# Performance work log

Hardware: AMD Instinct MI355X
Metric: run time of the kernel (lower is better)

The kernel has to match this reference:

```python
import jax, jax.numpy as jnp
import numpy as np

N_NODES = 2000
C_IN = 64
G_DIMS = [1, 256, 256, 256]
C_EMB = 128
HAZ = 512


def setup_inputs() -> dict:
    key = jax.random.key(0)
    ks = jax.random.split(key, 16)
    B, E = 128, 64000
    inp = jax.random.normal(ks[0], (B, C_IN + N_NODES), dtype=jnp.float32)
    src = jax.random.randint(ks[1], (E,), 0, N_NODES, dtype=jnp.int32)
    dst = jax.random.randint(ks[2], (E,), 0, N_NODES, dtype=jnp.int32)
    def lin(k, fi, fo):
        return jax.random.normal(k, (fi, fo), dtype=jnp.float32) / np.sqrt(fi)
    params = {
        'W0': lin(ks[3], G_DIMS[0], G_DIMS[1]), 'b0': jnp.zeros((G_DIMS[1],), jnp.float32),
        'W1': lin(ks[4], G_DIMS[1], G_DIMS[2]), 'b1': jnp.zeros((G_DIMS[2],), jnp.float32),
        'W2': lin(ks[5], G_DIMS[2], G_DIMS[3]), 'b2': jnp.zeros((G_DIMS[3],), jnp.float32),
        'We': lin(ks[6], C_IN, C_EMB),
        'Wh1': lin(ks[7], 2 * G_DIMS[3] + C_EMB, HAZ), 'bh1': jnp.zeros((HAZ,), jnp.float32),
        'Wh2': lin(ks[8], HAZ, HAZ // 2), 'bh2': jnp.zeros((HAZ // 2,), jnp.float32),
        'Wh3': lin(ks[9], HAZ // 2, 1),
    }
    return dict(inp=inp, src=src, dst=dst, **params)


def _gcn_layer(x, src, dst, dout_is, din_is, W, b):
    # x: [B, N, d_in]; DGL GraphConv norm='both': D_out^-1/2 gather-sum D_in^-1/2, then XW+b
    B, N, _ = x.shape
    h = x * dout_is[None, :, None]
    msg = h[:, src, :]                                   # [B, E, d_in]
    agg = jnp.zeros_like(h).at[:, dst, :].add(msg)       # scatter-add over edges
    agg = agg * din_is[None, :, None]
    return agg @ W + b


def reference(inp, src, dst, W0, b0, W1, b1, W2, b2, We, Wh1, bh1, Wh2, bh2, Wh3):
    B = inp.shape[0]
    inp_c = inp[:, :C_IN]
    x = inp[:, C_IN:].reshape(B, N_NODES, 1)
    # degree normalizers (DGL clamps degree to min 1)
    ones = jnp.ones_like(src, dtype=jnp.float32)
    dout = jnp.maximum(jnp.zeros((N_NODES,), jnp.float32).at[src].add(ones), 1.0)
    din = jnp.maximum(jnp.zeros((N_NODES,), jnp.float32).at[dst].add(ones), 1.0)
    dout_is = jax.lax.rsqrt(dout)
    din_is = jax.lax.rsqrt(din)

    embed = jax.nn.relu(inp_c @ We)
    hg = 0.0
    for W, b in ((W0, b0), (W1, b1), (W2, b2)):
        x = jax.nn.relu(_gcn_layer(x, src, dst, dout_is, din_is, W, b))
        r = jnp.concatenate([x.mean(axis=1), x.max(axis=1)], axis=-1)  # avg|max readout
        hg = hg + jax.nn.relu(r)

    fusion = jnp.concatenate([embed, hg], axis=1)
    h = jax.nn.relu(fusion @ Wh1 + bh1)
    h = jax.nn.relu(h @ Wh2 + bh2)
    out = h @ Wh3  # out_dim == 1 -> Identity head (dropout=0 / eval)
    return out
```

## Files before the change

### kernel.cpp

```cpp
#include <hip/hip_runtime.h>
#include <hip/hip_bf16.h>

#define B_    128
#define NN    2000
#define C_    256
#define E_    64000
#define CIN   64
#define ROWST 2064
#define CEMB  128
#define HAZ1  512
#define HAZ2  256
#define FUSD  640

typedef unsigned short u16;
typedef __attribute__((ext_vector_type(8))) short short8;
typedef __attribute__((ext_vector_type(8))) unsigned short ush8;
typedef __attribute__((ext_vector_type(4))) float f32x4;

static constexpr size_t OFF_DEGO = 0;
static constexpr size_t OFF_DEGI = 8000;
static constexpr size_t OFF_CUR  = 16000;
static constexpr size_t OFF_WOUT = 24000;
static constexpr size_t OFF_WIN  = 32000;
static constexpr size_t OFF_IOFF = 40000;
static constexpr size_t OFF_CSRC = 48192;
static constexpr size_t OFF_CSRW = 304192;
static constexpr size_t OFF_HG   = 560192;
static constexpr size_t OFF_EMB  = 822336;
static constexpr size_t OFF_H1   = 887872;
static constexpr size_t OFF_H2   = 1150016;
static constexpr size_t OFF_PSUM = 1281088;
static constexpr size_t OFF_PMAX = 1412160;
static constexpr size_t OFF_A    = 1543232;
static constexpr size_t OFF_WT1H = 2567232;
static constexpr size_t OFF_WT2H = 2829376;
static constexpr size_t OFF_XBUF = 4194304;

__device__ __forceinline__ u16 f2bf(float f) {
    union { float f; unsigned u; } v; v.f = f;
    unsigned u = v.u;
    unsigned r = (u + 0x7FFFu + ((u >> 16) & 1u)) >> 16;
    return (u16)r;
}
__device__ __forceinline__ float bf2f(u16 h) {
    union { unsigned u; float f; } v; v.u = ((unsigned)h) << 16;
    return v.f;
}

__global__ void k_zero(float* p, int n) {
    int i = blockIdx.x * 256 + threadIdx.x;
    if (i < n) p[i] = 0.f;
}

__global__ void k_deg(const int* __restrict__ src, const int* __restrict__ dst,
                      int* __restrict__ dego, int* __restrict__ degi) {
    int e = blockIdx.x * 256 + threadIdx.x;
    if (e < E_) {
        atomicAdd(&dego[src[e]], 1);
        atomicAdd(&degi[dst[e]], 1);
    }
}

__global__ void k_norm(const int* __restrict__ dego, const int* __restrict__ degi,
                       float* __restrict__ wout, float* __restrict__ win) {
    int n = blockIdx.x * 256 + threadIdx.x;
    if (n < NN) {
        wout[n] = rsqrtf(fmaxf((float)dego[n], 1.f));
        win[n]  = rsqrtf(fmaxf((float)degi[n], 1.f));
    }
}

__global__ void k_scan(const int* __restrict__ degi, int* __restrict__ ioff) {
    __shared__ int part[512];
    int t = threadIdx.x;
    int base = t * 4;
    int v[4]; int s = 0;
#pragma unroll
    for (int i = 0; i < 4; i++) {
        int idx = base + i;
        v[i] = (idx < NN) ? degi[idx] : 0;
        s += v[i];
    }
    part[t] = s;
    __syncthreads();
    for (int o = 1; o < 512; o <<= 1) {
        int x = 0;
        if (t >= o) x = part[t - o];
        __syncthreads();
        part[t] += x;
        __syncthreads();
    }
    int run = (t == 0) ? 0 : part[t - 1];
#pragma unroll
    for (int i = 0; i < 4; i++) {
        int idx = base + i;
        if (idx <= NN) ioff[idx] = run;
        run += v[i];
    }
}

__global__ void k_fill(const int* __restrict__ src, const int* __restrict__ dst,
                       const float* __restrict__ wout, const float* __restrict__ win,
                       const int* __restrict__ ioff, int* __restrict__ cursor,
                       int* __restrict__ csrc, float* __restrict__ csrw) {
    int e = blockIdx.x * 256 + threadIdx.x;
    if (e < E_) {
        int d = dst[e];
        int s = src[e];
        int p = atomicAdd(&cursor[d], 1);
        int i = ioff[d] + p;
        csrc[i] = s;
        csrw[i] = wout[s] * win[d];
    }
}

__global__ __launch_bounds__(256) void k_prepw(const float* __restrict__ W,
                                               u16* __restrict__ Th) {
    int n = blockIdx.x, k = threadIdx.x;
    Th[n * 256 + k] = f2bf(W[(size_t)k * 256 + n]);
}

__global__ __launch_bounds__(64) void k_agg_scalar(
        const float* __restrict__ inp, const int* __restrict__ ioff,
        const int* __restrict__ csrc, const float* __restrict__ csrw,
        float* __restrict__ a) {
    int n = blockIdx.x * 64 + threadIdx.x;
    int b = blockIdx.y;
    if (n >= NN) return;
    const float* row = inp + (size_t)b * ROWST + CIN;
    int e0 = ioff[n], e1 = ioff[n + 1];
    float acc = 0.f;
    for (int i = e0; i < e1; i++) acc += csrw[i] * row[csrc[i]];
    a[(size_t)b * NN + n] = acc;
}

__global__ __launch_bounds__(256) void k_pool0(
        const float* __restrict__ a, const float* __restrict__ W0,
        const float* __restrict__ b0, float* __restrict__ hg) {
    int b = blockIdx.x, c = threadIdx.x;
    float w0c = W0[c], b0c = b0[c];
    const float* ab = a + (size_t)b * NN;
    float s = 0.f, mx = 0.f;
    for (int n = 0; n < NN; n++) {
        float v = fmaxf(fmaf(ab[n], w0c, b0c), 0.f);
        s += v;
        mx = fmaxf(mx, v);
    }
    hg[(size_t)b * 512 + c]       += s * (1.f / (float)NN);
    hg[(size_t)b * 512 + 256 + c] += mx;
}

__global__ __launch_bounds__(64) void k_agg_l1(
        const float* __restrict__ a, const int* __restrict__ ioff,
        const int* __restrict__ csrc, const float* __restrict__ csrw,
        const float* __restrict__ W0, const float* __restrict__ b0,
        u16* __restrict__ xout, int b0g) {
    int n = blockIdx.x, bp = blockIdx.y, t = threadIdx.x;
    int half = t >> 5, c8 = (t & 31) * 8;
    int bl = bp * 2 + half;
    int e0 = ioff[n], e1 = ioff[n + 1];
    const float* ab = a + (size_t)(b0g + bl) * NN;
    float w[8], bb[8], acca[8] = {}, accb[8] = {};
#pragma unroll
    for (int j = 0; j < 8; j++) { w[j] = W0[c8 + j]; bb[j] = b0[c8 + j]; }
    int i = e0;
    for (; i + 2 <= e1; i += 2) {
        float a0 = ab[csrc[i]],     we0 = csrw[i];
        float a1 = ab[csrc[i + 1]], we1 = csrw[i + 1];
#pragma unroll
        for (int j = 0; j < 8; j++) {
            acca[j] = fmaf(fmaxf(fmaf(a0, w[j], bb[j]), 0.f), we0, acca[j]);
            accb[j] = fmaf(fmaxf(fmaf(a1, w[j], bb[j]), 0.f), we1, accb[j]);
        }
    }
    if (i < e1) {
        float a0 = ab[csrc[i]], we0 = csrw[i];
#pragma unroll
        for (int j = 0; j < 8; j++)
            acca[j] = fmaf(fmaxf(fmaf(a0, w[j], bb[j]), 0.f), we0, acca[j]);
    }
    ush8 o;
#pragma unroll
    for (int j = 0; j < 8; j++) o[j] = f2bf(acca[j] + accb[j]);
    *reinterpret_cast<ush8*>(&xout[((size_t)bl * NN + n) * C_ + c8]) = o;
}

__global__ __launch_bounds__(64) void k_agg_bf(
        const u16* __restrict__ xin, const int* __restrict__ ioff,
        const int* __restrict__ csrc, const float* __restrict__ csrw,
        u16* __restrict__ xout, int QBH) {
    int l = blockIdx.x + NN * blockIdx.y;
    int xcd = l & 7, slot = l >> 3;
    int q = slot / NN;
    int bp = xcd * QBH + q;
    int n = slot - q * NN;
    int t = threadIdx.x;
    int half = t >> 5, c8 = (t & 31) * 8;
    int bl = bp * 2 + half;
    int e0 = ioff[n], e1 = ioff[n + 1];
    const u16* xb = xin + (size_t)bl * NN * C_ + c8;
    float acca[8] = {}, accb[8] = {};
    int i = e0;
    for (; i + 2 <= e1; i += 2) {
        int s0 = csrc[i];     float w0 = csrw[i];
        int s1 = csrc[i + 1]; float w1 = csrw[i + 1];
        ush8 v0 = *reinterpret_cast<const ush8*>(&xb[(size_t)s0 * C_]);
        ush8 v1 = *reinterpret_cast<const ush8*>(&xb[(size_t)s1 * C_]);
#pragma unroll
        for (int j = 0; j < 8; j++) {
            acca[j] = fmaf(bf2f(v0[j]), w0, acca[j]);
            accb[j] = fmaf(bf2f(v1[j]), w1, accb[j]);
        }
    }
    if (i < e1) {
        int s0 = csrc[i]; float w0 = csrw[i];
        ush8 v0 = *reinterpret_cast<const ush8*>(&xb[(size_t)s0 * C_]);
#pragma unroll
        for (int j = 0; j < 8; j++) acca[j] = fmaf(bf2f(v0[j]), w0, acca[j]);
    }
    ush8 o;
#pragma unroll
    for (int j = 0; j < 8; j++) o[j] = f2bf(acca[j] + accb[j]);
    *reinterpret_cast<ush8*>(&xout[((size_t)bl * NN + n) * C_ + c8]) = o;
}

#define GM 128
#define GN 128
#define GK 32
#define LDP 40

template<int OUT>
__global__ __launch_bounds__(256) void k_gemm_mfma(
        const u16* __restrict__ Abf, const u16* __restrict__ WTh,
        const float* __restrict__ bias,
        u16* __restrict__ Cbf, float* __restrict__ psum, float* __restrict__ pmax) {
    __shared__ u16 Ah[GM * LDP];
    __shared__ u16 Bh[GN * LDP];
    __shared__ float lsum[2][2][GN];
    __shared__ float lmax[2][2][GN];
    int tid  = threadIdx.x;
    int lane = tid & 63, wave = tid >> 6;
    int wm = wave >> 1, wn = wave & 1;
    int n0 = blockIdx.x * GN;
    int m0 = blockIdx.y * GM;
    int blk = lane >> 4, rr = lane & 15;

    f32x4 acc[4][4] = {};

    for (int k0 = 0; k0 < 256; k0 += GK) {
#pragma unroll
        for (int q = 0; q < 2; q++) {
            int f = tid + 256 * q;
            int row = f >> 2, seg = f & 3;
            ush8 va = *reinterpret_cast<const ush8*>(
                &Abf[(size_t)(m0 + row) * 256 + k0 + seg * 8]);
            ush8 vb = *reinterpret_cast<const ush8*>(
                &WTh[(size_t)(n0 + row) * 256 + k0 + seg * 8]);
            *reinterpret_cast<ush8*>(&Ah[row * LDP + seg * 8]) = va;
            *reinterpret_cast<ush8*>(&Bh[row * LDP + seg * 8]) = vb;
        }
        __syncthreads();

        short8 af[4], bf[4];
#pragma unroll
        for (int mr = 0; mr < 4; mr++)
            af[mr] = *reinterpret_cast<const short8*>(
                &Ah[(wm * 64 + mr * 16 + rr) * LDP + blk * 8]);
#pragma unroll
        for (int nr = 0; nr < 4; nr++)
            bf[nr] = *reinterpret_cast<const short8*>(
                &Bh[(wn * 64 + nr * 16 + rr) * LDP + blk * 8]);
#pragma unroll
        for (int mr = 0; mr < 4; mr++)
#pragma unroll
            for (int nr = 0; nr < 4; nr++)
                acc[mr][nr] = __builtin_amdgcn_mfma_f32_16x16x32_bf16(
                    af[mr], bf[nr], acc[mr][nr], 0, 0, 0);
        __syncthreads();
    }

    int bl0   = m0 / NN;
    int split = (bl0 + 1) * NN - m0;

    float s_lo[4] = {}, s_hi[4] = {}, m_lo[4] = {}, m_hi[4] = {};
#pragma unroll
    for (int nr = 0; nr < 4; nr++) {
        int col = n0 + wn * 64 + nr * 16 + rr;
        float bs = bias[col];
#pragma unroll
        for (int mr = 0; mr < 4; mr++) {
            int rl = wm * 64 + mr * 16 + blk * 4;
#pragma unroll
            for (int j = 0; j < 4; j++) {
                float v = fmaxf(acc[mr][nr][j] + bs, 0.f);
                if (OUT == 1)
                    Cbf[(size_t)(m0 + rl + j) * 256 + col] = f2bf(v);
                bool second = (rl + j) >= split;
                s_lo[nr] += second ? 0.f : v;
                s_hi[nr] += second ? v : 0.f;
                m_lo[nr] = second ? m_lo[nr] : fmaxf(m_lo[nr], v);
                m_hi[nr] = second ? fmaxf(m_hi[nr], v) : m_hi[nr];
            }
        }
    }
#pragma unroll
    for (int nr = 0; nr < 4; nr++) {
        s_lo[nr] += __shfl_xor(s_lo[nr], 16); s_lo[nr] += __shfl_xor(s_lo[nr], 32);
        s_hi[nr] += __shfl_xor(s_hi[nr], 16); s_hi[nr] += __shfl_xor(s_hi[nr], 32);
        m_lo[nr] = fmaxf(m_lo[nr], __shfl_xor(m_lo[nr], 16));
        m_lo[nr] = fmaxf(m_lo[nr], __shfl_xor(m_lo[nr], 32));
        m_hi[nr] = fmaxf(m_hi[nr], __shfl_xor(m_hi[nr], 16));
        m_hi[nr] = fmaxf(m_hi[nr], __shfl_xor(m_hi[nr], 32));
    }
    if (lane < 16) {
#pragma unroll
        for (int nr = 0; nr < 4; nr++) {
            int cl = wn * 64 + nr * 16 + lane;
            lsum[0][wm][cl] = s_lo[nr];
            lsum[1][wm][cl] = s_hi[nr];
            lmax[0][wm][cl] = m_lo[nr];
            lmax[1][wm][cl] = m_hi[nr];
        }
    }
    __syncthreads();
    {
        int seg = tid >> 7, cl = tid & 127;
        if (!(seg == 1 && split >= GM)) {
            float s = lsum[seg][0][cl] + lsum[seg][1][cl];
            float m = fmaxf(lmax[seg][0][cl], lmax[seg][1][cl]);
            int blx = bl0 + seg;
            atomicAdd(&psum[blx * C_ + n0 + cl], s);
            atomicMax((unsigned int*)&pmax[blx * C_ + n0 + cl], __float_as_uint(m));
        }
    }
}

__global__ __launch_bounds__(256) void k_pool_combine(
        float* __restrict__ psum, float* __restrict__ pmax,
        float* __restrict__ hg, int b0g) {
    int bl = blockIdx.x, c = threadIdx.x;
    float s = psum[bl * C_ + c];
    float m = pmax[bl * C_ + c];
    psum[bl * C_ + c] = 0.f;
    pmax[bl * C_ + c] = 0.f;
    size_t b = b0g + bl;
    hg[b * 512 + c]       += s * (1.f / (float)NN);
    hg[b * 512 + 256 + c] += m;
}

__global__ __launch_bounds__(128) void k_embed(
        const float* __restrict__ inp, const float* __restrict__ We,
        float* __restrict__ emb) {
    int b = blockIdx.x, c = threadIdx.x;
    const float* row = inp + (size_t)b * ROWST;
    float a = 0.f;
    for (int k = 0; k < CIN; k++) a += row[k] * We[k * CEMB + c];
    emb[b * CEMB + c] = fmaxf(a, 0.f);
}

__global__ __launch_bounds__(512) void k_mlp1(
        const float* __restrict__ emb, const float* __restrict__ hg,
        const float* __restrict__ Wh1, const float* __restrict__ bh1,
        float* __restrict__ h1) {
    __shared__ float fus[FUSD];
    int b = blockIdx.x, j = threadIdx.x;
    if (j < CEMB) fus[j] = emb[b * CEMB + j];
    fus[CEMB + j] = hg[(size_t)b * 512 + j];
    __syncthreads();
    float a = bh1[j];
    for (int k = 0; k < FUSD; k++) a += fus[k] * Wh1[(size_t)k * HAZ1 + j];
    h1[(size_t)b * HAZ1 + j] = fmaxf(a, 0.f);
}

__global__ __launch_bounds__(256) void k_mlp2(
        const float* __restrict__ h1, const float* __restrict__ Wh2,
        const float* __restrict__ bh2, float* __restrict__ h2) {
    __shared__ float f2[HAZ1];
    int b = blockIdx.x, j = threadIdx.x;
    f2[j]       = h1[(size_t)b * HAZ1 + j];
    f2[256 + j] = h1[(size_t)b * HAZ1 + 256 + j];
    __syncthreads();
    float a = bh2[j];
    for (int k = 0; k < HAZ1; k++) a += f2[k] * Wh2[(size_t)k * HAZ2 + j];
    h2[(size_t)b * HAZ2 + j] = fmaxf(a, 0.f);
}

__global__ __launch_bounds__(256) void k_out(
        const float* __restrict__ h2, const float* __restrict__ Wh3,
        float* __restrict__ out) {
    __shared__ float red[256];
    int b = blockIdx.x, t = threadIdx.x;
    red[t] = h2[(size_t)b * HAZ2 + t] * Wh3[t];
    __syncthreads();
    for (int o = 128; o > 0; o >>= 1) {
        if (t < o) red[t] += red[t + o];
        __syncthreads();
    }
    if (t == 0) out[b] = red[0];
}

extern "C" void kernel_launch(void* const* d_in, const int* in_sizes, int n_in,
                              void* d_out, int out_size, void* d_ws, size_t ws_size,
                              hipStream_t stream) {
    const float* inp = (const float*)d_in[0];
    const int*   src = (const int*)d_in[1];
    const int*   dst = (const int*)d_in[2];
    const float* W0  = (const float*)d_in[3];
    const float* b0  = (const float*)d_in[4];
    const float* W1  = (const float*)d_in[5];
    const float* b1  = (const float*)d_in[6];
    const float* W2  = (const float*)d_in[7];
    const float* b2  = (const float*)d_in[8];
    const float* We  = (const float*)d_in[9];
    const float* Wh1 = (const float*)d_in[10];
    const float* bh1 = (const float*)d_in[11];
    const float* Wh2 = (const float*)d_in[12];
    const float* bh2 = (const float*)d_in[13];
    const float* Wh3 = (const float*)d_in[14];
    float* out = (float*)d_out;

    char* ws = (char*)d_ws;
    int*   dego = (int*)(ws + OFF_DEGO);
    int*   degi = (int*)(ws + OFF_DEGI);
    int*   cur  = (int*)(ws + OFF_CUR);
    float* wout = (float*)(ws + OFF_WOUT);
    float* win  = (float*)(ws + OFF_WIN);
    int*   ioff = (int*)(ws + OFF_IOFF);
    int*   csrc = (int*)(ws + OFF_CSRC);
    float* csrw = (float*)(ws + OFF_CSRW);
    float* hg   = (float*)(ws + OFF_HG);
    float* emb  = (float*)(ws + OFF_EMB);
    float* h1   = (float*)(ws + OFF_H1);
    float* h2   = (float*)(ws + OFF_H2);
    float* psum = (float*)(ws + OFF_PSUM);
    float* pmax = (float*)(ws + OFF_PMAX);
    float* avec = (float*)(ws + OFF_A);
    u16*   wt1h = (u16*)(ws + OFF_WT1H);
    u16*   wt2h = (u16*)(ws + OFF_WT2H);

    const size_t perb = (size_t)NN * C_ * 4;
    int CB = 128;
    while (CB > 16 && OFF_XBUF + (size_t)CB * perb > ws_size) CB >>= 1;
    int nchunk = B_ / CB;
    int CBH = CB / 2;
    int QBH = CBH / 8;

    u16* xB   = (u16*)(ws + OFF_XBUF);
    u16* xAbf = (u16*)(ws + OFF_XBUF + (size_t)CB * NN * C_ * 2);

    k_zero<<<dim3((6000 + 255) / 256), 256, 0, stream>>>((float*)dego, 6000);
    k_zero<<<dim3((65536 + 255) / 256), 256, 0, stream>>>(hg, 65536);
    k_zero<<<dim3((65536 + 255) / 256), 256, 0, stream>>>(psum, 65536);

    k_deg<<<dim3((E_ + 255) / 256), 256, 0, stream>>>(src, dst, dego, degi);
    k_norm<<<dim3((NN + 255) / 256), 256, 0, stream>>>(dego, degi, wout, win);
    k_scan<<<1, 512, 0, stream>>>(degi, ioff);
    k_fill<<<dim3((E_ + 255) / 256), 256, 0, stream>>>(src, dst, wout, win, ioff, cur, csrc, csrw);
    k_prepw<<<256, 256, 0, stream>>>(W1, wt1h);
    k_prepw<<<256, 256, 0, stream>>>(W2, wt2h);

    k_agg_scalar<<<dim3((NN + 63) / 64, B_), 64, 0, stream>>>(inp, ioff, csrc, csrw, avec);
    k_pool0<<<B_, 256, 0, stream>>>(avec, W0, b0, hg);

    dim3 gridNB(NN, CBH);
    dim3 gridGemm(C_ / GN, (CB * NN) / GM);

    for (int c = 0; c < nchunk; ++c) {
        int b0g = c * CB;

        k_agg_l1<<<gridNB, 64, 0, stream>>>(avec, ioff, csrc, csrw, W0, b0, xB, b0g);
        k_gemm_mfma<1><<<gridGemm, 256, 0, stream>>>(xB, wt1h, b1, xAbf, psum, pmax);
        k_pool_combine<<<CB, 256, 0, stream>>>(psum, pmax, hg, b0g);

        k_agg_bf<<<gridNB, 64, 0, stream>>>(xAbf, ioff, csrc, csrw, xB, QBH);
        k_gemm_mfma<0><<<gridGemm, 256, 0, stream>>>(xB, wt2h, b2, nullptr, psum, pmax);
        k_pool_combine<<<CB, 256, 0, stream>>>(psum, pmax, hg, b0g);
    }

    k_embed<<<B_, 128, 0, stream>>>(inp, We, emb);
    k_mlp1<<<B_, 512, 0, stream>>>(emb, hg, Wh1, bh1, h1);
    k_mlp2<<<B_, 256, 0, stream>>>(h1, Wh2, bh2, h2);
    k_out<<<B_, 256, 0, stream>>>(h2, Wh3, out);
}
```

Before: 645.2 us.

## Fuse small kernels, transpose input for aggregation, prefetch GEMM tiles, unroll gather

Merges the zero, norm/scan, prepw, embed/mlp and out kernels into fewer launches. It transposes the node input to node-major [N,B] so scalar aggregation and layer-1 gathers read coalesced across the batch. The bf16 aggregation loop is unrolled to four edges, and the MFMA GEMM register-prefetches the next K tile while computing the current one. These target launch overhead, uncoalesced gathers and memory latency, at the cost of an extra transpose kernel and workspace buffer.

```diff
diff --git a/kernel.cpp b/kernel.cpp
--- a/kernel.cpp
+++ b/kernel.cpp
@@ -26,14 +26,13 @@
 static constexpr size_t OFF_CSRC = 48192;
 static constexpr size_t OFF_CSRW = 304192;
 static constexpr size_t OFF_HG   = 560192;
-static constexpr size_t OFF_EMB  = 822336;
 static constexpr size_t OFF_H1   = 887872;
-static constexpr size_t OFF_H2   = 1150016;
 static constexpr size_t OFF_PSUM = 1281088;
 static constexpr size_t OFF_PMAX = 1412160;
 static constexpr size_t OFF_A    = 1543232;
 static constexpr size_t OFF_WT1H = 2567232;
 static constexpr size_t OFF_WT2H = 2829376;
+static constexpr size_t OFF_XT   = 3091520;
 static constexpr size_t OFF_XBUF = 4194304;
 
 __device__ __forceinline__ u16 f2bf(float f) {
@@ -47,9 +46,12 @@
     return v.f;
 }
 
-__global__ void k_zero(float* p, int n) {
+__global__ void k_init(int* __restrict__ deg3, float* __restrict__ hg,
+                       float* __restrict__ ps) {
     int i = blockIdx.x * 256 + threadIdx.x;
-    if (i < n) p[i] = 0.f;
+    if (i < 6000) deg3[i] = 0;
+    else if (i < 6000 + 65536) hg[i - 6000] = 0.f;
+    else if (i < 6000 + 131072) ps[i - 71536] = 0.f;
 }
 
 __global__ void k_deg(const int* __restrict__ src, const int* __restrict__ dst,
@@ -61,16 +63,9 @@
     }
 }
 
-__global__ void k_norm(const int* __restrict__ dego, const int* __restrict__ degi,
-                       float* __restrict__ wout, float* __restrict__ win) {
-    int n = blockIdx.x * 256 + threadIdx.x;
-    if (n < NN) {
-        wout[n] = rsqrtf(fmaxf((float)dego[n], 1.f));
-        win[n]  = rsqrtf(fmaxf((float)degi[n], 1.f));
-    }
-}
-
-__global__ void k_scan(const int* __restrict__ degi, int* __restrict__ ioff) {
+__global__ void k_scan_norm(const int* __restrict__ degi, const int* __restrict__ dego,
+                            int* __restrict__ ioff, float* __restrict__ wout,
+                            float* __restrict__ win) {
     __shared__ int part[512];
     int t = threadIdx.x;
     int base = t * 4;
@@ -79,6 +74,10 @@
     for (int i = 0; i < 4; i++) {
         int idx = base + i;
         v[i] = (idx < NN) ? degi[idx] : 0;
+        if (idx < NN) {
+            wout[idx] = rsqrtf(fmaxf((float)dego[idx], 1.f));
+            win[idx]  = rsqrtf(fmaxf((float)v[i], 1.f));
+        }
         s += v[i];
     }
     part[t] = s;
@@ -114,35 +113,61 @@
     }
 }
 
-__global__ __launch_bounds__(256) void k_prepw(const float* __restrict__ W,
-                                               u16* __restrict__ Th) {
-    int n = blockIdx.x, k = threadIdx.x;
-    Th[n * 256 + k] = f2bf(W[(size_t)k * 256 + n]);
-}
-
-__global__ __launch_bounds__(64) void k_agg_scalar(
-        const float* __restrict__ inp, const int* __restrict__ ioff,
+__global__ __launch_bounds__(256) void k_prepw2(
+        const float* __restrict__ W1, const float* __restrict__ W2,
+        u16* __restrict__ T1, u16* __restrict__ T2) {
+    int which = blockIdx.x >> 8;
+    int n = blockIdx.x & 255, k = threadIdx.x;
+    const float* W = which ? W2 : W1;
+    u16* T = which ? T2 : T1;
+    T[n * 256 + k] = f2bf(W[(size_t)k * 256 + n]);
+}
+
+__global__ __launch_bounds__(256) void k_xt(
+        const float* __restrict__ inp, float* __restrict__ xT) {
+    __shared__ float tl[32][33];
+    int tx = threadIdx.x & 31, ty = threadIdx.x >> 5;
+    int n0 = blockIdx.x * 32, b0 = blockIdx.y * 32;
+#pragma unroll
+    for (int r = 0; r < 4; r++) {
+        int b = b0 + ty + r * 8;
+        int n = n0 + tx;
+        if (n < NN) tl[tx][ty + r * 8] = inp[(size_t)b * ROWST + CIN + n];
+    }
+    __syncthreads();
+#pragma unroll
+    for (int r = 0; r < 4; r++) {
+        int n = n0 + ty + r * 8;
+        int b = b0 + tx;
+        if (n < NN) xT[(size_t)n * B_ + b] = tl[ty + r * 8][tx];
+    }
+}
+
+__global__ __launch_bounds__(64) void k_agg_scalar_t(
+        const float* __restrict__ xT, const int* __restrict__ ioff,
         const int* __restrict__ csrc, const float* __restrict__ csrw,
-        float* __restrict__ a) {
-    int n = blockIdx.x * 64 + threadIdx.x;
-    int b = blockIdx.y;
-    if (n >= NN) return;
-    const float* row = inp + (size_t)b * ROWST + CIN;
+        float* __restrict__ aT) {
+    int n = blockIdx.x;
+    int b = blockIdx.y * 64 + threadIdx.x;
     int e0 = ioff[n], e1 = ioff[n + 1];
-    float acc = 0.f;
-    for (int i = e0; i < e1; i++) acc += csrw[i] * row[csrc[i]];
-    a[(size_t)b * NN + n] = acc;
+    float acc0 = 0.f, acc1 = 0.f;
+    int i = e0;
+    for (; i + 2 <= e1; i += 2) {
+        acc0 = fmaf(csrw[i],     xT[(size_t)csrc[i] * B_ + b],     acc0);
+        acc1 = fmaf(csrw[i + 1], xT[(size_t)csrc[i + 1] * B_ + b], acc1);
+    }
+    if (i < e1) acc0 = fmaf(csrw[i], xT[(size_t)csrc[i] * B_ + b], acc0);
+    aT[(size_t)n * B_ + b] = acc0 + acc1;
 }
 
 __global__ __launch_bounds__(256) void k_pool0(
-        const float* __restrict__ a, const float* __restrict__ W0,
+        const float* __restrict__ aT, const float* __restrict__ W0,
         const float* __restrict__ b0, float* __restrict__ hg) {
     int b = blockIdx.x, c = threadIdx.x;
     float w0c = W0[c], b0c = b0[c];
-    const float* ab = a + (size_t)b * NN;
     float s = 0.f, mx = 0.f;
     for (int n = 0; n < NN; n++) {
-        float v = fmaxf(fmaf(ab[n], w0c, b0c), 0.f);
+        float v = fmaxf(fmaf(aT[(size_t)n * B_ + b], w0c, b0c), 0.f);
         s += v;
         mx = fmaxf(mx, v);
     }
@@ -151,22 +176,30 @@
 }
 
 __global__ __launch_bounds__(64) void k_agg_l1(
-        const float* __restrict__ a, const int* __restrict__ ioff,
+        const float* __restrict__ aT, const int* __restrict__ ioff,
         const int* __restrict__ csrc, const float* __restrict__ csrw,
         const float* __restrict__ W0, const float* __restrict__ b0,
         u16* __restrict__ xout, int b0g) {
     int n = blockIdx.x, bp = blockIdx.y, t = threadIdx.x;
     int half = t >> 5, c8 = (t & 31) * 8;
     int bl = bp * 2 + half;
+    int bg = b0g + bl;
     int e0 = ioff[n], e1 = ioff[n + 1];
-    const float* ab = a + (size_t)(b0g + bl) * NN;
     float w[8], bb[8], acca[8] = {}, accb[8] = {};
-#pragma unroll
-    for (int j = 0; j < 8; j++) { w[j] = W0[c8 + j]; bb[j] = b0[c8 + j]; }
+    {
+        float4 w0 = *reinterpret_cast<const float4*>(&W0[c8]);
+        float4 w1 = *reinterpret_cast<const float4*>(&W0[c8 + 4]);
+        float4 v0 = *reinterpret_cast<const float4*>(&b0[c8]);
+        float4 v1 = *reinterpret_cast<const float4*>(&b0[c8 + 4]);
+        w[0]=w0.x; w[1]=w0.y; w[2]=w0.z; w[3]=w0.w;
+        w[4]=w1.x; w[5]=w1.y; w[6]=w1.z; w[7]=w1.w;
+        bb[0]=v0.x; bb[1]=v0.y; bb[2]=v0.z; bb[3]=v0.w;
+        bb[4]=v1.x; bb[5]=v1.y; bb[6]=v1.z; bb[7]=v1.w;
+    }
     int i = e0;
     for (; i + 2 <= e1; i += 2) {
-        float a0 = ab[csrc[i]],     we0 = csrw[i];
-        float a1 = ab[csrc[i + 1]], we1 = csrw[i + 1];
+        float a0 = aT[(size_t)csrc[i] * B_ + bg],     we0 = csrw[i];
+        float a1 = aT[(size_t)csrc[i + 1] * B_ + bg], we1 = csrw[i + 1];
 #pragma unroll
         for (int j = 0; j < 8; j++) {
             acca[j] = fmaf(fmaxf(fmaf(a0, w[j], bb[j]), 0.f), we0, acca[j]);
@@ -174,7 +207,7 @@
         }
     }
     if (i < e1) {
-        float a0 = ab[csrc[i]], we0 = csrw[i];
+        float a0 = aT[(size_t)csrc[i] * B_ + bg], we0 = csrw[i];
 #pragma unroll
         for (int j = 0; j < 8; j++)
             acca[j] = fmaf(fmaxf(fmaf(a0, w[j], bb[j]), 0.f), we0, acca[j]);
@@ -199,20 +232,26 @@
     int bl = bp * 2 + half;
     int e0 = ioff[n], e1 = ioff[n + 1];
     const u16* xb = xin + (size_t)bl * NN * C_ + c8;
-    float acca[8] = {}, accb[8] = {};
+    float acca[8] = {}, accb[8] = {}, accc[8] = {}, accd[8] = {};
     int i = e0;
-    for (; i + 2 <= e1; i += 2) {
+    for (; i + 4 <= e1; i += 4) {
         int s0 = csrc[i];     float w0 = csrw[i];
         int s1 = csrc[i + 1]; float w1 = csrw[i + 1];
+        int s2 = csrc[i + 2]; float w2 = csrw[i + 2];
+        int s3 = csrc[i + 3]; float w3 = csrw[i + 3];
         ush8 v0 = *reinterpret_cast<const ush8*>(&xb[(size_t)s0 * C_]);
         ush8 v1 = *reinterpret_cast<const ush8*>(&xb[(size_t)s1 * C_]);
+        ush8 v2 = *reinterpret_cast<const ush8*>(&xb[(size_t)s2 * C_]);
+        ush8 v3 = *reinterpret_cast<const ush8*>(&xb[(size_t)s3 * C_]);
 #pragma unroll
         for (int j = 0; j < 8; j++) {
             acca[j] = fmaf(bf2f(v0[j]), w0, acca[j]);
             accb[j] = fmaf(bf2f(v1[j]), w1, accb[j]);
-        }
-    }
-    if (i < e1) {
+            accc[j] = fmaf(bf2f(v2[j]), w2, accc[j]);
+            accd[j] = fmaf(bf2f(v3[j]), w3, accd[j]);
+        }
+    }
+    for (; i < e1; ++i) {
         int s0 = csrc[i]; float w0 = csrw[i];
         ush8 v0 = *reinterpret_cast<const ush8*>(&xb[(size_t)s0 * C_]);
 #pragma unroll
@@ -220,7 +259,8 @@
     }
     ush8 o;
 #pragma unroll
-    for (int j = 0; j < 8; j++) o[j] = f2bf(acca[j] + accb[j]);
+    for (int j = 0; j < 8; j++)
+        o[j] = f2bf((acca[j] + accb[j]) + (accc[j] + accd[j]));
     *reinterpret_cast<ush8*>(&xout[((size_t)bl * NN + n) * C_ + c8]) = o;
 }
 
@@ -244,23 +284,30 @@
     int n0 = blockIdx.x * GN;
     int m0 = blockIdx.y * GM;
     int blk = lane >> 4, rr = lane & 15;
+    int sr0 = tid >> 2, sseg = (tid & 3) * 8;
+    int sr1 = sr0 + 64;
 
     f32x4 acc[4][4] = {};
 
-    for (int k0 = 0; k0 < 256; k0 += GK) {
-#pragma unroll
-        for (int q = 0; q < 2; q++) {
-            int f = tid + 256 * q;
-            int row = f >> 2, seg = f & 3;
-            ush8 va = *reinterpret_cast<const ush8*>(
-                &Abf[(size_t)(m0 + row) * 256 + k0 + seg * 8]);
-            ush8 vb = *reinterpret_cast<const ush8*>(
-                &WTh[(size_t)(n0 + row) * 256 + k0 + seg * 8]);
-            *reinterpret_cast<ush8*>(&Ah[row * LDP + seg * 8]) = va;
-            *reinterpret_cast<ush8*>(&Bh[row * LDP + seg * 8]) = vb;
-        }
+    ush8 va0 = *reinterpret_cast<const ush8*>(&Abf[(size_t)(m0 + sr0) * 256 + sseg]);
+    ush8 vb0 = *reinterpret_cast<const ush8*>(&WTh[(size_t)(n0 + sr0) * 256 + sseg]);
+    ush8 va1 = *reinterpret_cast<const ush8*>(&Abf[(size_t)(m0 + sr1) * 256 + sseg]);
+    ush8 vb1 = *reinterpret_cast<const ush8*>(&WTh[(size_t)(n0 + sr1) * 256 + sseg]);
+
+#pragma unroll
+    for (int kk = 0; kk < 8; kk++) {
+        *reinterpret_cast<ush8*>(&Ah[sr0 * LDP + sseg]) = va0;
+        *reinterpret_cast<ush8*>(&Bh[sr0 * LDP + sseg]) = vb0;
+        *reinterpret_cast<ush8*>(&Ah[sr1 * LDP + sseg]) = va1;
+        *reinterpret_cast<ush8*>(&Bh[sr1 * LDP + sseg]) = vb1;
         __syncthreads();
-
+        if (kk < 7) {
+            int k0n = (kk + 1) * GK;
+            va0 = *reinterpret_cast<const ush8*>(&Abf[(size_t)(m0 + sr0) * 256 + k0n + sseg]);
+            vb0 = *reinterpret_cast<const ush8*>(&WTh[(size_t)(n0 + sr0) * 256 + k0n + sseg]);
+            va1 = *reinterpret_cast<const ush8*>(&Abf[(size_t)(m0 + sr1) * 256 + k0n + sseg]);
+            vb1 = *reinterpret_cast<const ush8*>(&WTh[(size_t)(n0 + sr1) * 256 + k0n + sseg]);
+        }
         short8 af[4], bf[4];
 #pragma unroll
         for (int mr = 0; mr < 4; mr++)
@@ -348,23 +395,18 @@
     hg[b * 512 + 256 + c] += m;
 }
 
-__global__ __launch_bounds__(128) void k_embed(
+__global__ __launch_bounds__(512) void k_mlp1f(
         const float* __restrict__ inp, const float* __restrict__ We,
-        float* __restrict__ emb) {
-    int b = blockIdx.x, c = threadIdx.x;
-    const float* row = inp + (size_t)b * ROWST;
-    float a = 0.f;
-    for (int k = 0; k < CIN; k++) a += row[k] * We[k * CEMB + c];
-    emb[b * CEMB + c] = fmaxf(a, 0.f);
-}
-
-__global__ __launch_bounds__(512) void k_mlp1(
-        const float* __restrict__ emb, const float* __restrict__ hg,
-        const float* __restrict__ Wh1, const float* __restrict__ bh1,
-        float* __restrict__ h1) {
+        const float* __restrict__ hg, const float* __restrict__ Wh1,
+        const float* __restrict__ bh1, float* __restrict__ h1) {
     __shared__ float fus[FUSD];
     int b = blockIdx.x, j = threadIdx.x;
-    if (j < CEMB) fus[j] = emb[b * CEMB + j];
+    if (j < CEMB) {
+        const float* row = inp + (size_t)b * ROWST;
+        float a = 0.f;
+        for (int k = 0; k < CIN; k++) a += row[k] * We[k * CEMB + j];
+        fus[j] = fmaxf(a, 0.f);
+    }
     fus[CEMB + j] = hg[(size_t)b * 512 + j];
     __syncthreads();
     float a = bh1[j];
@@ -372,31 +414,25 @@
     h1[(size_t)b * HAZ1 + j] = fmaxf(a, 0.f);
 }
 
-__global__ __launch_bounds__(256) void k_mlp2(
+__global__ __launch_bounds__(256) void k_mlp2out(
         const float* __restrict__ h1, const float* __restrict__ Wh2,
-        const float* __restrict__ bh2, float* __restrict__ h2) {
+        const float* __restrict__ bh2, const float* __restrict__ Wh3,
+        float* __restrict__ out) {
     __shared__ float f2[HAZ1];
+    __shared__ float red[256];
     int b = blockIdx.x, j = threadIdx.x;
     f2[j]       = h1[(size_t)b * HAZ1 + j];
     f2[256 + j] = h1[(size_t)b * HAZ1 + 256 + j];
     __syncthreads();
     float a = bh2[j];
     for (int k = 0; k < HAZ1; k++) a += f2[k] * Wh2[(size_t)k * HAZ2 + j];
-    h2[(size_t)b * HAZ2 + j] = fmaxf(a, 0.f);
-}
-
-__global__ __launch_bounds__(256) void k_out(
-        const float* __restrict__ h2, const float* __restrict__ Wh3,
-        float* __restrict__ out) {
-    __shared__ float red[256];
-    int b = blockIdx.x, t = threadIdx.x;
-    red[t] = h2[(size_t)b * HAZ2 + t] * Wh3[t];
+    red[j] = fmaxf(a, 0.f) * Wh3[j];
     __syncthreads();
     for (int o = 128; o > 0; o >>= 1) {
-        if (t < o) red[t] += red[t + o];
+        if (j < o) red[j] += red[j + o];
         __syncthreads();
     }
-    if (t == 0) out[b] = red[0];
+    if (j == 0) out[b] = red[0];
 }
 
 extern "C" void kernel_launch(void* const* d_in, const int* in_sizes, int n_in,
@@ -429,12 +465,11 @@
     int*   csrc = (int*)(ws + OFF_CSRC);
     float* csrw = (float*)(ws + OFF_CSRW);
     float* hg   = (float*)(ws + OFF_HG);
-    float* emb  = (float*)(ws + OFF_EMB);
     float* h1   = (float*)(ws + OFF_H1);
-    float* h2   = (float*)(ws + OFF_H2);
     float* psum = (float*)(ws + OFF_PSUM);
     float* pmax = (float*)(ws + OFF_PMAX);
-    float* avec = (float*)(ws + OFF_A);
+    float* aT   = (float*)(ws + OFF_A);
+    float* xT   = (float*)(ws + OFF_XT);
     u16*   wt1h = (u16*)(ws + OFF_WT1H);
     u16*   wt2h = (u16*)(ws + OFF_WT2H);
 
@@ -448,19 +483,15 @@
     u16* xB   = (u16*)(ws + OFF_XBUF);
     u16* xAbf = (u16*)(ws + OFF_XBUF + (size_t)CB * NN * C_ * 2);
 
-    k_zero<<<dim3((6000 + 255) / 256), 256, 0, stream>>>((float*)dego, 6000);
-    k_zero<<<dim3((65536 + 255) / 256), 256, 0, stream>>>(hg, 65536);
-    k_zero<<<dim3((65536 + 255) / 256), 256, 0, stream>>>(psum, 65536);
-
+    k_init<<<dim3(536), 256, 0, stream>>>(dego, hg, psum);
     k_deg<<<dim3((E_ + 255) / 256), 256, 0, stream>>>(src, dst, dego, degi);
-    k_norm<<<dim3((NN + 255) / 256), 256, 0, stream>>>(dego, degi, wout, win);
-    k_scan<<<1, 512, 0, stream>>>(degi, ioff);
+    k_scan_norm<<<1, 512, 0, stream>>>(degi, dego, ioff, wout, win);
     k_fill<<<dim3((E_ + 255) / 256), 256, 0, stream>>>(src, dst, wout, win, ioff, cur, csrc, csrw);
-    k_prepw<<<256, 256, 0, stream>>>(W1, wt1h);
-    k_prepw<<<256, 256, 0, stream>>>(W2, wt2h);
-
-    k_agg_scalar<<<dim3((NN + 63) / 64, B_), 64, 0, stream>>>(inp, ioff, csrc, csrw, avec);
-    k_pool0<<<B_, 256, 0, stream>>>(avec, W0, b0, hg);
+    k_prepw2<<<dim3(512), 256, 0, stream>>>(W1, W2, wt1h, wt2h);
+    k_xt<<<dim3(63, 4), 256, 0, stream>>>(inp, xT);
+
+    k_agg_scalar_t<<<dim3(NN, 2), 64, 0, stream>>>(xT, ioff, csrc, csrw, aT);
+    k_pool0<<<B_, 256, 0, stream>>>(aT, W0, b0, hg);
 
     dim3 gridNB(NN, CBH);
     dim3 gridGemm(C_ / GN, (CB * NN) / GM);
@@ -468,7 +499,7 @@
     for (int c = 0; c < nchunk; ++c) {
         int b0g = c * CB;
 
-        k_agg_l1<<<gridNB, 64, 0, stream>>>(avec, ioff, csrc, csrw, W0, b0, xB, b0g);
+        k_agg_l1<<<gridNB, 64, 0, stream>>>(aT, ioff, csrc, csrw, W0, b0, xB, b0g);
         k_gemm_mfma<1><<<gridGemm, 256, 0, stream>>>(xB, wt1h, b1, xAbf, psum, pmax);
         k_pool_combine<<<CB, 256, 0, stream>>>(psum, pmax, hg, b0g);
 
@@ -477,8 +508,6 @@
         k_pool_combine<<<CB, 256, 0, stream>>>(psum, pmax, hg, b0g);
     }
 
-    k_embed<<<B_, 128, 0, stream>>>(inp, We, emb);
-    k_mlp1<<<B_, 512, 0, stream>>>(emb, hg, Wh1, bh1, h1);
-    k_mlp2<<<B_, 256, 0, stream>>>(h1, Wh2, bh2, h2);
-    k_out<<<B_, 256, 0, stream>>>(h2, Wh3, out);
-}
+    k_mlp1f<<<B_, 512, 0, stream>>>(inp, We, hg, Wh1, bh1, h1);
+    k_mlp2out<<<B_, 256, 0, stream>>>(h1, Wh2, bh2, Wh3, out);
+}
```

After: 626.4 us (median of 2 runs). 2.9% less time.
